# Kernel tuning notes

Measured on AMD Instinct MI355X. Metric: run time of the kernel, lower is better.

## Reference

```python
import jax, jax.numpy as jnp
import numpy as np

N = 100000
M = 20000
NNZ = 1000000
D_IN = 128
D_OUT = 128


def setup_inputs() -> dict:
    key = jax.random.key(0)
    ks = jax.random.split(key, 6)
    return {
        "node_features": jax.random.normal(ks[0], (N, D_IN), dtype=jnp.float32),
        "data": jax.random.uniform(ks[1], (NNZ,), dtype=jnp.float32),
        "W": jax.random.normal(ks[2], (D_OUT, D_IN), dtype=jnp.float32) / np.sqrt(D_IN),
        "b": jax.random.normal(ks[3], (D_OUT,), dtype=jnp.float32),
        "v_idx": jax.random.randint(ks[4], (NNZ,), 0, N, dtype=jnp.int32),
        "e_idx": jax.random.randint(ks[5], (NNZ,), 0, M, dtype=jnp.int32),
        "n": N,
        "m": M,
    }


def reference(node_features, data, W, b, v_idx, e_idx, n, m):
    # Linear projection (eqx.nn.Linear: y = W @ x + b, vmapped over nodes)
    x = node_features @ W.T + b  # [n, d_out]

    # Degree normalization terms
    d_e = jax.ops.segment_sum(data, e_idx, num_segments=m)  # [m]
    d_v = jax.ops.segment_sum(data, v_idx, num_segments=n)  # [n]
    d_e_inv = jnp.where(d_e > 0, 1.0 / d_e, 0.0)
    d_v_inv = jnp.where(d_v > 0, 1.0 / d_v, 0.0)

    # vertex -> edge: H.T @ x via gather-scale-scatter
    e = jax.ops.segment_sum(x[v_idx] * data[:, None], e_idx, num_segments=m)  # [m, d_out]
    e = e * d_e_inv[:, None]

    # edge -> vertex: H @ e via gather-scale-scatter
    out = jax.ops.segment_sum(e[e_idx] * data[:, None], v_idx, num_segments=n)  # [n, d_out]
    out = out * d_v_inv[:, None]
    return out
```

## Files before the change

### kernel.cpp

```cpp
#include <hip/hip_runtime.h>

#define DF  128
#define NB  128
#define ME  20000
#define EW  10000
#define VW  16667
#define VP  3

typedef float f32x2 __attribute__((ext_vector_type(2)));

__device__ __forceinline__ unsigned bf16rne(float f) {
    unsigned u = __float_as_uint(f);
    return (u + 0x7fffu + ((u >> 16) & 1u)) >> 16;
}

__device__ __forceinline__ unsigned w15enc(float f) {
    unsigned bits = __float_as_uint(f);
    unsigned r = (bits + 0xFFFu + ((bits >> 13) & 1u)) >> 13;
    return (r > (96u << 10)) ? (r - (96u << 10)) : 0u;
}
__device__ __forceinline__ float w15dec(unsigned w) {
    return w ? __uint_as_float((w + (96u << 10)) << 13) : 0.f;
}

#if __has_builtin(__builtin_amdgcn_fdot2_f32_bf16)
typedef __bf16 bf16x2 __attribute__((ext_vector_type(2)));
__device__ __forceinline__ float dot2bf(unsigned a, unsigned b, float c) {
    return __builtin_amdgcn_fdot2_f32_bf16(
        __builtin_bit_cast(bf16x2, a), __builtin_bit_cast(bf16x2, b), c, false);
}
#else
__device__ __forceinline__ float dot2bf(unsigned a, unsigned b, float c) {
    c += __uint_as_float(a << 16) * __uint_as_float(b << 16);
    c += __uint_as_float(a & 0xffff0000u) * __uint_as_float(b & 0xffff0000u);
    return c;
}
#endif

__global__ __launch_bounds__(256) void hist_lds(
    const int* __restrict__ vi, const int* __restrict__ ei,
    unsigned short* __restrict__ rank,
    unsigned* __restrict__ bhE, unsigned* __restrict__ bhV, int nnz, int epb)
{
    __shared__ unsigned lh[VW];
    int b = blockIdx.x;
    int lo = b * epb;
    int hi = min(nnz, lo + epb);
    int iters = epb >> 10;

    for (int w = threadIdx.x; w < EW; w += 256) lh[w] = 0;
    __syncthreads();
    for (int it = 0; it < iters; ++it) {
        int i = lo + (it * 256 + threadIdx.x) * 4;
        if (i + 4 <= hi) {
            int4 e4 = *(const int4*)(ei + i);
            int ee[4] = {e4.x, e4.y, e4.z, e4.w};
            unsigned short r[4];
            #pragma unroll
            for (int q = 0; q < 4; ++q) {
                int sh = (ee[q] & 1) * 16;
                unsigned ret = atomicAdd(&lh[ee[q] >> 1], 1u << sh);
                r[q] = (unsigned short)((ret >> sh) & 0xffffu);
            }
            *(ushort4*)(rank + i) = ushort4{r[0], r[1], r[2], r[3]};
        } else {
            for (int j = i; j < hi; ++j) {
                int e = ei[j]; int sh = (e & 1) * 16;
                unsigned ret = atomicAdd(&lh[e >> 1], 1u << sh);
                rank[j] = (unsigned short)((ret >> sh) & 0xffffu);
            }
        }
    }
    __syncthreads();
    for (int w = threadIdx.x; w < EW; w += 256)
        bhE[(size_t)b * EW + w] = lh[w];

    for (int p = 0; p < VP; ++p) {
        int vbase = p * (2 * VW);
        __syncthreads();
        for (int w = threadIdx.x; w < VW; w += 256) lh[w] = 0;
        __syncthreads();
        for (int it = 0; it < iters; ++it) {
            int i = lo + (it * 256 + threadIdx.x) * 4;
            if (i + 4 <= hi) {
                int4 v4 = *(const int4*)(vi + i);
                int vv[4] = {v4.x, v4.y, v4.z, v4.w};
                #pragma unroll
                for (int q = 0; q < 4; ++q) {
                    int d = vv[q] - vbase;
                    if (d >= 0 && d < 2 * VW)
                        atomicAdd(&lh[d >> 1], 1u << ((d & 1) * 16));
                }
            } else {
                for (int j = i; j < hi; ++j) {
                    int d = vi[j] - vbase;
                    if (d >= 0 && d < 2 * VW)
                        atomicAdd(&lh[d >> 1], 1u << ((d & 1) * 16));
                }
            }
        }
        __syncthreads();
        for (int w = threadIdx.x; w < VW; w += 256)
            bhV[(size_t)b * (VP * VW) + p * VW + w] = lh[w];
    }
}

__global__ __launch_bounds__(256) void scan_cols_conv(
    unsigned* __restrict__ bhE, const unsigned* __restrict__ bhV,
    int* __restrict__ totE, int* __restrict__ totV,
    const float* __restrict__ nf, const float* __restrict__ W,
    unsigned* __restrict__ nfh, unsigned* __restrict__ wp, int n, int n64)
{
    int tid = blockIdx.x * 256 + threadIdx.x;
    if (tid < EW) {
        unsigned run0 = 0, run1 = 0;
        #pragma unroll 4
        for (int b = 0; b < NB; ++b) {
            unsigned w = bhE[(size_t)b * EW + tid];
            unsigned c0 = w & 0xffffu, c1 = w >> 16;
            bhE[(size_t)b * EW + tid] = run0 | (run1 << 16);
            run0 += c0; run1 += c1;
        }
        totE[2 * tid] = (int)run0;
        totE[2 * tid + 1] = (int)run1;
    } else if (tid < EW + VP * VW) {
        int w = tid - EW;
        unsigned s0 = 0, s1 = 0;
        #pragma unroll 4
        for (int b = 0; b < NB; ++b) {
            unsigned x = bhV[(size_t)b * (VP * VW) + w];
            s0 += x & 0xffffu; s1 += x >> 16;
        }
        int p = w / VW, wi = w - p * VW;
        int k0 = p * (2 * VW) + 2 * wi;
        if (k0 < n) totV[k0] = (int)s0;
        if (k0 + 1 < n) totV[k0 + 1] = (int)s1;
    }
    int nth = gridDim.x * 256;
    const float2* __restrict__ in2 = (const float2*)nf;
    for (int i = tid; i < n64; i += nth) {
        float2 f = in2[i];
        nfh[i] = bf16rne(f.x) | (bf16rne(f.y) << 16);
    }
    if (tid < DF * 64) {
        int j = tid >> 6, k2 = tid & 63;
        float2 f = ((const float2*)W)[tid];
        wp[k2 * DF + j] = bf16rne(f.x) | (bf16rne(f.y) << 16);
    }
}

__global__ __launch_bounds__(256) void scan_k1(
    const int* __restrict__ totE, const int* __restrict__ totV,
    int* __restrict__ bsum, int m, int len)
{
    __shared__ int s[256];
    int tid = threadIdx.x;
    int base = blockIdx.x * 2048 + tid * 8;
    int t = 0;
    #pragma unroll
    for (int i = 0; i < 8; ++i) {
        int idx = base + i;
        if (idx < len) t += (idx < m) ? totE[idx] : totV[idx - m];
    }
    s[tid] = t; __syncthreads();
    for (int d = 128; d > 0; d >>= 1) {
        if (tid < d) s[tid] += s[tid + d];
        __syncthreads();
    }
    if (tid == 0) bsum[blockIdx.x] = s[0];
}

__global__ __launch_bounds__(256) void scan_k2(int* __restrict__ bsum, int nb)
{
    __shared__ int s[256];
    int t = threadIdx.x;
    int v = (t < nb) ? bsum[t] : 0;
    s[t] = v; __syncthreads();
    for (int d = 1; d < 256; d <<= 1) {
        int u = (t >= d) ? s[t - d] : 0;
        __syncthreads();
        s[t] += u;
        __syncthreads();
    }
    if (t < nb) bsum[t] = s[t] - v;
}

__global__ __launch_bounds__(256) void scan_k3(
    const int* __restrict__ totE, const int* __restrict__ totV,
    const int* __restrict__ bsum, int* __restrict__ seg, int m, int len)
{
    __shared__ int s[256];
    int tid = threadIdx.x;
    int base = blockIdx.x * 2048 + tid * 8;
    int v[8]; int t = 0;
    #pragma unroll
    for (int i = 0; i < 8; ++i) {
        int idx = base + i;
        v[i] = (idx < len) ? ((idx < m) ? totE[idx] : totV[idx - m]) : 0;
        t += v[i];
    }
    s[tid] = t; __syncthreads();
    for (int d = 1; d < 256; d <<= 1) {
        int u = (tid >= d) ? s[tid - d] : 0;
        __syncthreads();
        s[tid] += u;
        __syncthreads();
    }
    int run = bsum[blockIdx.x] + (s[tid] - t);
    #pragma unroll
    for (int i = 0; i < 8; ++i) {
        int idx = base + i;
        if (idx < len) { seg[idx] = run; run += v[i]; }
    }
}

__global__ __launch_bounds__(256) void place_kernel(
    const int* __restrict__ vi, const int* __restrict__ ei,
    const float* __restrict__ data, const unsigned short* __restrict__ rank,
    int* __restrict__ seg, const unsigned* __restrict__ bhE,
    unsigned* __restrict__ pair, int nnz, int m, int epb)
{
    int base = (blockIdx.x * 256 + threadIdx.x) * 4;
    if (base + 4 <= nnz) {
        int bH = base / epb;
        const unsigned* __restrict__ bb = bhE + (size_t)bH * EW;
        int4 e4 = *(const int4*)(ei + base);
        int4 v4 = *(const int4*)(vi + base);
        ushort4 r4 = *(const ushort4*)(rank + base);
        float4 d4 = *(const float4*)(data + base);
        int ee[4] = {e4.x, e4.y, e4.z, e4.w};
        int vv[4] = {v4.x, v4.y, v4.z, v4.w};
        unsigned short rr[4] = {r4.x, r4.y, r4.z, r4.w};
        float dd[4] = {d4.x, d4.y, d4.z, d4.w};
        #pragma unroll
        for (int q = 0; q < 4; ++q) {
            unsigned w15 = w15enc(dd[q]) << 17;
            unsigned bword = bb[ee[q] >> 1];
            int baseE = (int)((bword >> ((ee[q] & 1) * 16)) & 0xffffu);
            int pe = seg[ee[q]] + baseE + rr[q];
            int pv = atomicAdd(&seg[m + vv[q]], 1);
            __builtin_nontemporal_store(w15 | (unsigned)vv[q], pair + pe);
            __builtin_nontemporal_store(w15 | (unsigned)ee[q], pair + pv);
        }
    } else {
        for (int i = base; i < nnz; ++i) {
            int e = ei[i], v = vi[i];
            unsigned w15 = w15enc(data[i]) << 17;
            unsigned bword = bhE[(size_t)(i / epb) * EW + (e >> 1)];
            int baseE = (int)((bword >> ((e & 1) * 16)) & 0xffffu);
            int pe = seg[e] + baseE + rank[i];
            int pv = atomicAdd(&seg[m + v], 1);
            __builtin_nontemporal_store(w15 | (unsigned)v, pair + pe);
            __builtin_nontemporal_store(w15 | (unsigned)e, pair + pv);
        }
    }
}

__global__ __launch_bounds__(256) void gather_y_linear(
    const unsigned* __restrict__ nfh, const int* __restrict__ seg,
    const unsigned* __restrict__ pair, const unsigned* __restrict__ wp,
    const float* __restrict__ b, unsigned* __restrict__ e16, int m, int nnz)
{
    __shared__ unsigned rowbuf[4][64];
    int wv = threadIdx.x >> 6;
    int wid = (blockIdx.x * 256 + threadIdx.x) >> 6;
    int lane = threadIdx.x & 63;
    if (wid >= m) return;
    int start = seg[wid];
    int end   = (wid == m - 1) ? nnz : seg[wid + 1];
    float ax = 0.f, ay = 0.f, ws = 0.f;
    int k = start;
    for (; k + 16 <= end; k += 16) {
        unsigned p[16];
        #pragma unroll
        for (int q = 0; q < 16; ++q) p[q] = __builtin_nontemporal_load(pair + k + q);
        unsigned u[16];
        #pragma unroll
        for (int q = 0; q < 16; ++q) u[q] = nfh[(size_t)(p[q] & 0x1FFFFu) * 64 + lane];
        #pragma unroll
        for (int q = 0; q < 16; ++q) {
            float w = w15dec(p[q] >> 17);
            ax += w * __uint_as_float(u[q] << 16);
            ay += w * __uint_as_float(u[q] & 0xffff0000u);
            ws += w;
        }
    }
    for (; k + 4 <= end; k += 4) {
        unsigned p[4];
        #pragma unroll
        for (int q = 0; q < 4; ++q) p[q] = __builtin_nontemporal_load(pair + k + q);
        unsigned u[4];
        #pragma unroll
        for (int q = 0; q < 4; ++q) u[q] = nfh[(size_t)(p[q] & 0x1FFFFu) * 64 + lane];
        #pragma unroll
        for (int q = 0; q < 4; ++q) {
            float w = w15dec(p[q] >> 17);
            ax += w * __uint_as_float(u[q] << 16);
            ay += w * __uint_as_float(u[q] & 0xffff0000u);
            ws += w;
        }
    }
    for (; k < end; ++k) {
        unsigned p0 = __builtin_nontemporal_load(pair + k);
        float w0 = w15dec(p0 >> 17);
        unsigned ua = nfh[(size_t)(p0 & 0x1FFFFu) * 64 + lane];
        ax += w0 * __uint_as_float(ua << 16);
        ay += w0 * __uint_as_float(ua & 0xffff0000u);
        ws += w0;
    }
    float inv = (ws > 0.f) ? 1.f / ws : 0.f;
    rowbuf[wv][lane] = bf16rne(ax * inv) | (bf16rne(ay * inv) << 16);

    float2 bb = ((const float2*)b)[lane];
    float acc0 = (ws > 0.f) ? bb.x : 0.f;
    float acc1 = (ws > 0.f) ? bb.y : 0.f;
    const unsigned* __restrict__ row = rowbuf[wv];
    #pragma unroll 8
    for (int k2 = 0; k2 < 64; ++k2) {
        unsigned r = row[k2];
        uint2 u = ((const uint2*)(wp + k2 * DF))[lane];
        acc0 = dot2bf(r, u.x, acc0);
        acc1 = dot2bf(r, u.y, acc1);
    }
    e16[(size_t)wid * 64 + lane] = bf16rne(acc0) | (bf16rne(acc1) << 16);
}

__global__ __launch_bounds__(256) void gather_out(
    const unsigned* __restrict__ e16, const int* __restrict__ seg,
    const unsigned* __restrict__ pair,
    float* __restrict__ out, int n, int m, int nnz)
{
    int wid = (blockIdx.x * 256 + threadIdx.x) >> 6;
    int lane = threadIdx.x & 63;
    if (wid >= n) return;
    int start = wid ? seg[m + wid - 1] : nnz;
    int end   = seg[m + wid];
    float ax = 0.f, ay = 0.f, ws = 0.f;
    int k = start;
    for (; k + 16 <= end; k += 16) {
        unsigned p[16];
        #pragma unroll
        for (int q = 0; q < 16; ++q) p[q] = __builtin_nontemporal_load(pair + k + q);
        unsigned u[16];
        #pragma unroll
        for (int q = 0; q < 16; ++q) u[q] = e16[(size_t)(p[q] & 0x1FFFFu) * 64 + lane];
        #pragma unroll
        for (int q = 0; q < 16; ++q) {
            float w = w15dec(p[q] >> 17);
            ax += w * __uint_as_float(u[q] << 16);
            ay += w * __uint_as_float(u[q] & 0xffff0000u);
            ws += w;
        }
    }
    for (; k + 4 <= end; k += 4) {
        unsigned p[4];
        #pragma unroll
        for (int q = 0; q < 4; ++q) p[q] = __builtin_nontemporal_load(pair + k + q);
        unsigned u[4];
        #pragma unroll
        for (int q = 0; q < 4; ++q) u[q] = e16[(size_t)(p[q] & 0x1FFFFu) * 64 + lane];
        #pragma unroll
        for (int q = 0; q < 4; ++q) {
            float w = w15dec(p[q] >> 17);
            ax += w * __uint_as_float(u[q] << 16);
            ay += w * __uint_as_float(u[q] & 0xffff0000u);
            ws += w;
        }
    }
    for (; k < end; ++k) {
        unsigned p0 = __builtin_nontemporal_load(pair + k);
        float w0 = w15dec(p0 >> 17);
        unsigned ua = e16[(size_t)(p0 & 0x1FFFFu) * 64 + lane];
        ax += w0 * __uint_as_float(ua << 16);
        ay += w0 * __uint_as_float(ua & 0xffff0000u);
        ws += w0;
    }
    float inv = (ws > 0.f) ? 1.f / ws : 0.f;
    f32x2 o = {ax * inv, ay * inv};
    __builtin_nontemporal_store(o, (f32x2*)out + (size_t)wid * 64 + lane);
}

extern "C" void kernel_launch(void* const* d_in, const int* in_sizes, int n_in,
                              void* d_out, int out_size, void* d_ws, size_t ws_size,
                              hipStream_t stream)
{
    const float* nf   = (const float*)d_in[0];
    const float* data = (const float*)d_in[1];
    const float* W    = (const float*)d_in[2];
    const float* b    = (const float*)d_in[3];
    const int*   vi   = (const int*)d_in[4];
    const int*   ei   = (const int*)d_in[5];

    const int n   = in_sizes[0] / DF;
    const int nnz = in_sizes[1];
    const int m   = ME;

    const int epb = ((nnz + NB - 1) / NB + 1023) & ~1023;

    int*   seg   = (int*)d_ws;
    int*   bsum  = seg + (m + n);
    int*   totE  = bsum + 256;
    int*   totV  = totE + m;
    unsigned short* rank = (unsigned short*)(totV + n);
    unsigned* pair = (unsigned*)(rank + nnz);
    unsigned* e16 = pair + 2 * (size_t)nnz;
    unsigned* wp  = e16 + (size_t)m * 64;
    unsigned* nfh = wp + DF * 64;
    unsigned* bhE = nfh + (size_t)n * 64;
    unsigned* bhV = bhE + (size_t)NB * EW;
    float* out   = (float*)d_out;

    hist_lds<<<NB, 256, 0, stream>>>(vi, ei, rank, bhE, bhV, nnz, epb);

    scan_cols_conv<<<512, 256, 0, stream>>>(bhE, bhV, totE, totV,
                                            nf, W, nfh, wp, n, n * 64);

    int len = m + n;
    int nb = (len + 2047) / 2048;
    scan_k1<<<nb, 256, 0, stream>>>(totE, totV, bsum, m, len);
    scan_k2<<<1, 256, 0, stream>>>(bsum, nb);
    scan_k3<<<nb, 256, 0, stream>>>(totE, totV, bsum, seg, m, len);

    int nbQ = (nnz / 4 + 255) / 256;
    place_kernel<<<nbQ, 256, 0, stream>>>(vi, ei, data, rank, seg, bhE,
                                          pair, nnz, m, epb);

    gather_y_linear<<<(m + 3) / 4, 256, 0, stream>>>(nfh, seg, pair, wp, b,
                                                     e16, m, nnz);
    gather_out<<<(n + 3) / 4, 256, 0, stream>>>(e16, seg, pair, out, n, m, nnz);
}
```

Measured before the change: 266.7 us.

## Replace global atomic vertex placement with per-block rank-based counting sort

The vertex-side histogram pass now records each entry's rank within its block, and the column scan turns the vertex block histograms into exclusive per-block offsets. The placement kernel then computes each vertex-sorted position deterministically from the segment start, block offset and rank, instead of a global atomicAdd on the segment counter. This removes about a million contended global atomics and makes the vertex order deterministic. In exchange it adds an extra rank array write and read and an in-place scan of bhV, and e16 now aliases the rank buffers to save workspace. Segment end handling in both gather kernels is adjusted because seg is no longer advanced by atomics.

```diff
diff --git a/kernel.cpp b/kernel.cpp
--- a/kernel.cpp
+++ b/kernel.cpp
@@ -6,6 +6,7 @@
 #define EW  10000
 #define VW  16667
 #define VP  3
+#define VSPAN (2 * VW)
 
 typedef float f32x2 __attribute__((ext_vector_type(2)));
 
@@ -39,7 +40,7 @@
 
 __global__ __launch_bounds__(256) void hist_lds(
     const int* __restrict__ vi, const int* __restrict__ ei,
-    unsigned short* __restrict__ rank,
+    unsigned short* __restrict__ rankE, unsigned short* __restrict__ rankV,
     unsigned* __restrict__ bhE, unsigned* __restrict__ bhV, int nnz, int epb)
 {
     __shared__ unsigned lh[VW];
@@ -62,12 +63,12 @@
                 unsigned ret = atomicAdd(&lh[ee[q] >> 1], 1u << sh);
                 r[q] = (unsigned short)((ret >> sh) & 0xffffu);
             }
-            *(ushort4*)(rank + i) = ushort4{r[0], r[1], r[2], r[3]};
+            *(ushort4*)(rankE + i) = ushort4{r[0], r[1], r[2], r[3]};
         } else {
             for (int j = i; j < hi; ++j) {
                 int e = ei[j]; int sh = (e & 1) * 16;
                 unsigned ret = atomicAdd(&lh[e >> 1], 1u << sh);
-                rank[j] = (unsigned short)((ret >> sh) & 0xffffu);
+                rankE[j] = (unsigned short)((ret >> sh) & 0xffffu);
             }
         }
     }
@@ -76,7 +77,7 @@
         bhE[(size_t)b * EW + w] = lh[w];
 
     for (int p = 0; p < VP; ++p) {
-        int vbase = p * (2 * VW);
+        int vbase = p * VSPAN;
         __syncthreads();
         for (int w = threadIdx.x; w < VW; w += 256) lh[w] = 0;
         __syncthreads();
@@ -88,14 +89,20 @@
                 #pragma unroll
                 for (int q = 0; q < 4; ++q) {
                     int d = vv[q] - vbase;
-                    if (d >= 0 && d < 2 * VW)
-                        atomicAdd(&lh[d >> 1], 1u << ((d & 1) * 16));
+                    if (d >= 0 && d < VSPAN) {
+                        int sh = (d & 1) * 16;
+                        unsigned ret = atomicAdd(&lh[d >> 1], 1u << sh);
+                        rankV[i + q] = (unsigned short)((ret >> sh) & 0xffffu);
+                    }
                 }
             } else {
                 for (int j = i; j < hi; ++j) {
                     int d = vi[j] - vbase;
-                    if (d >= 0 && d < 2 * VW)
-                        atomicAdd(&lh[d >> 1], 1u << ((d & 1) * 16));
+                    if (d >= 0 && d < VSPAN) {
+                        int sh = (d & 1) * 16;
+                        unsigned ret = atomicAdd(&lh[d >> 1], 1u << sh);
+                        rankV[j] = (unsigned short)((ret >> sh) & 0xffffu);
+                    }
                 }
             }
         }
@@ -106,7 +113,7 @@
 }
 
 __global__ __launch_bounds__(256) void scan_cols_conv(
-    unsigned* __restrict__ bhE, const unsigned* __restrict__ bhV,
+    unsigned* __restrict__ bhE, unsigned* __restrict__ bhV,
     int* __restrict__ totE, int* __restrict__ totV,
     const float* __restrict__ nf, const float* __restrict__ W,
     unsigned* __restrict__ nfh, unsigned* __restrict__ wp, int n, int n64)
@@ -117,24 +124,24 @@
         #pragma unroll 4
         for (int b = 0; b < NB; ++b) {
             unsigned w = bhE[(size_t)b * EW + tid];
-            unsigned c0 = w & 0xffffu, c1 = w >> 16;
             bhE[(size_t)b * EW + tid] = run0 | (run1 << 16);
-            run0 += c0; run1 += c1;
+            run0 += w & 0xffffu; run1 += w >> 16;
         }
         totE[2 * tid] = (int)run0;
         totE[2 * tid + 1] = (int)run1;
     } else if (tid < EW + VP * VW) {
         int w = tid - EW;
-        unsigned s0 = 0, s1 = 0;
+        unsigned run0 = 0, run1 = 0;
         #pragma unroll 4
         for (int b = 0; b < NB; ++b) {
             unsigned x = bhV[(size_t)b * (VP * VW) + w];
-            s0 += x & 0xffffu; s1 += x >> 16;
+            bhV[(size_t)b * (VP * VW) + w] = run0 | (run1 << 16);
+            run0 += x & 0xffffu; run1 += x >> 16;
         }
         int p = w / VW, wi = w - p * VW;
-        int k0 = p * (2 * VW) + 2 * wi;
-        if (k0 < n) totV[k0] = (int)s0;
-        if (k0 + 1 < n) totV[k0 + 1] = (int)s1;
+        int k0 = p * VSPAN + 2 * wi;
+        if (k0 < n) totV[k0] = (int)run0;
+        if (k0 + 1 < n) totV[k0 + 1] = (int)run1;
     }
     int nth = gridDim.x * 256;
     const float2* __restrict__ in2 = (const float2*)nf;
@@ -216,40 +223,55 @@
 
 __global__ __launch_bounds__(256) void place_kernel(
     const int* __restrict__ vi, const int* __restrict__ ei,
-    const float* __restrict__ data, const unsigned short* __restrict__ rank,
-    int* __restrict__ seg, const unsigned* __restrict__ bhE,
+    const float* __restrict__ data,
+    const unsigned short* __restrict__ rankE,
+    const unsigned short* __restrict__ rankV,
+    const int* __restrict__ seg,
+    const unsigned* __restrict__ bhE, const unsigned* __restrict__ bhV,
     unsigned* __restrict__ pair, int nnz, int m, int epb)
 {
     int base = (blockIdx.x * 256 + threadIdx.x) * 4;
     if (base + 4 <= nnz) {
         int bH = base / epb;
-        const unsigned* __restrict__ bb = bhE + (size_t)bH * EW;
+        const unsigned* __restrict__ be = bhE + (size_t)bH * EW;
+        const unsigned* __restrict__ bv = bhV + (size_t)bH * (VP * VW);
         int4 e4 = *(const int4*)(ei + base);
         int4 v4 = *(const int4*)(vi + base);
-        ushort4 r4 = *(const ushort4*)(rank + base);
+        ushort4 re4 = *(const ushort4*)(rankE + base);
+        ushort4 rv4 = *(const ushort4*)(rankV + base);
         float4 d4 = *(const float4*)(data + base);
         int ee[4] = {e4.x, e4.y, e4.z, e4.w};
         int vv[4] = {v4.x, v4.y, v4.z, v4.w};
-        unsigned short rr[4] = {r4.x, r4.y, r4.z, r4.w};
+        unsigned short rre[4] = {re4.x, re4.y, re4.z, re4.w};
+        unsigned short rrv[4] = {rv4.x, rv4.y, rv4.z, rv4.w};
         float dd[4] = {d4.x, d4.y, d4.z, d4.w};
         #pragma unroll
         for (int q = 0; q < 4; ++q) {
             unsigned w15 = w15enc(dd[q]) << 17;
-            unsigned bword = bb[ee[q] >> 1];
-            int baseE = (int)((bword >> ((ee[q] & 1) * 16)) & 0xffffu);
-            int pe = seg[ee[q]] + baseE + rr[q];
-            int pv = atomicAdd(&seg[m + vv[q]], 1);
+            unsigned bwE = be[ee[q] >> 1];
+            int baseE = (int)((bwE >> ((ee[q] & 1) * 16)) & 0xffffu);
+            int p = vv[q] / VSPAN;
+            int d = vv[q] - p * VSPAN;
+            unsigned bwV = bv[p * VW + (d >> 1)];
+            int baseV = (int)((bwV >> ((d & 1) * 16)) & 0xffffu);
+            int pe = seg[ee[q]] + baseE + rre[q];
+            int pv = seg[m + vv[q]] + baseV + rrv[q];
             __builtin_nontemporal_store(w15 | (unsigned)vv[q], pair + pe);
             __builtin_nontemporal_store(w15 | (unsigned)ee[q], pair + pv);
         }
     } else {
         for (int i = base; i < nnz; ++i) {
+            int bH = i / epb;
             int e = ei[i], v = vi[i];
             unsigned w15 = w15enc(data[i]) << 17;
-            unsigned bword = bhE[(size_t)(i / epb) * EW + (e >> 1)];
-            int baseE = (int)((bword >> ((e & 1) * 16)) & 0xffffu);
-            int pe = seg[e] + baseE + rank[i];
-            int pv = atomicAdd(&seg[m + v], 1);
+            unsigned bwE = bhE[(size_t)bH * EW + (e >> 1)];
+            int baseE = (int)((bwE >> ((e & 1) * 16)) & 0xffffu);
+            int p = v / VSPAN;
+            int d = v - p * VSPAN;
+            unsigned bwV = bhV[(size_t)bH * (VP * VW) + p * VW + (d >> 1)];
+            int baseV = (int)((bwV >> ((d & 1) * 16)) & 0xffffu);
+            int pe = seg[e] + baseE + rankE[i];
+            int pv = seg[m + v] + baseV + rankV[i];
             __builtin_nontemporal_store(w15 | (unsigned)v, pair + pe);
             __builtin_nontemporal_store(w15 | (unsigned)e, pair + pv);
         }
@@ -259,7 +281,7 @@
 __global__ __launch_bounds__(256) void gather_y_linear(
     const unsigned* __restrict__ nfh, const int* __restrict__ seg,
     const unsigned* __restrict__ pair, const unsigned* __restrict__ wp,
-    const float* __restrict__ b, unsigned* __restrict__ e16, int m, int nnz)
+    const float* __restrict__ b, unsigned* __restrict__ e16, int m)
 {
     __shared__ unsigned rowbuf[4][64];
     int wv = threadIdx.x >> 6;
@@ -267,7 +289,7 @@
     int lane = threadIdx.x & 63;
     if (wid >= m) return;
     int start = seg[wid];
-    int end   = (wid == m - 1) ? nnz : seg[wid + 1];
+    int end   = seg[wid + 1];
     float ax = 0.f, ay = 0.f, ws = 0.f;
     int k = start;
     for (; k + 16 <= end; k += 16) {
@@ -328,13 +350,14 @@
 __global__ __launch_bounds__(256) void gather_out(
     const unsigned* __restrict__ e16, const int* __restrict__ seg,
     const unsigned* __restrict__ pair,
-    float* __restrict__ out, int n, int m, int nnz)
+    float* __restrict__ out, int n, int m, int tot)
 {
     int wid = (blockIdx.x * 256 + threadIdx.x) >> 6;
     int lane = threadIdx.x & 63;
     if (wid >= n) return;
-    int start = wid ? seg[m + wid - 1] : nnz;
-    int end   = seg[m + wid];
+    int idx = m + wid;
+    int start = seg[idx];
+    int end   = (wid == n - 1) ? tot : seg[idx + 1];
     float ax = 0.f, ay = 0.f, ws = 0.f;
     int k = start;
     for (; k + 16 <= end; k += 16) {
@@ -401,16 +424,18 @@
     int*   bsum  = seg + (m + n);
     int*   totE  = bsum + 256;
     int*   totV  = totE + m;
-    unsigned short* rank = (unsigned short*)(totV + n);
-    unsigned* pair = (unsigned*)(rank + nnz);
-    unsigned* e16 = pair + 2 * (size_t)nnz;
-    unsigned* wp  = e16 + (size_t)m * 64;
+    unsigned short* rankE = (unsigned short*)(totV + n);
+    unsigned short* rankV = rankE + nnz;
+    unsigned* e16 = (unsigned*)rankE;
+    unsigned* pair = (unsigned*)rankE + ((size_t)m * 64 > (size_t)nnz ?
+                     (size_t)m * 64 : (size_t)nnz);
+    unsigned* wp  = pair + 2 * (size_t)nnz;
     unsigned* nfh = wp + DF * 64;
     unsigned* bhE = nfh + (size_t)n * 64;
     unsigned* bhV = bhE + (size_t)NB * EW;
     float* out   = (float*)d_out;
 
-    hist_lds<<<NB, 256, 0, stream>>>(vi, ei, rank, bhE, bhV, nnz, epb);
+    hist_lds<<<NB, 256, 0, stream>>>(vi, ei, rankE, rankV, bhE, bhV, nnz, epb);
 
     scan_cols_conv<<<512, 256, 0, stream>>>(bhE, bhV, totE, totV,
                                             nf, W, nfh, wp, n, n * 64);
@@ -422,10 +447,9 @@
     scan_k3<<<nb, 256, 0, stream>>>(totE, totV, bsum, seg, m, len);
 
     int nbQ = (nnz / 4 + 255) / 256;
-    place_kernel<<<nbQ, 256, 0, stream>>>(vi, ei, data, rank, seg, bhE,
-                                          pair, nnz, m, epb);
-
-    gather_y_linear<<<(m + 3) / 4, 256, 0, stream>>>(nfh, seg, pair, wp, b,
-                                                     e16, m, nnz);
-    gather_out<<<(n + 3) / 4, 256, 0, stream>>>(e16, seg, pair, out, n, m, nnz);
-}
+    place_kernel<<<nbQ, 256, 0, stream>>>(vi, ei, data, rankE, rankV, seg,
+                                          bhE, bhV, pair, nnz, m, epb);
+
+    gather_y_linear<<<(m + 3) / 4, 256, 0, stream>>>(nfh, seg, pair, wp, b, e16, m);
+    gather_out<<<(n + 3) / 4, 256, 0, stream>>>(e16, seg, pair, out, n, m, 2 * nnz);
+}
```

Result: no change. 269.0 us (+0.9%).
